# Kernel optimization log

Measured on AMD Instinct MI355X. Metric: run time of the kernel, lower is better.

## Reference

```python
import jax, jax.numpy as jnp
import numpy as np

B, T, N, F = 32, 64, 128, 128
U, K1, K2 = 64, 64, 32
EPS = 1e-3  # keras BatchNormalization default epsilon
SLOPE = 0.01  # LeakyReLU negative_slope


def setup_inputs() -> dict:
    key = jax.random.key(0)
    ks = jax.random.split(key, 16)
    g = lambda k, sh, s=0.05: jax.random.normal(k, sh, dtype=jnp.float32) * s
    inp = {
        "x": jax.random.normal(ks[0], (B, T, F), dtype=jnp.float32),
        "a": jax.random.uniform(ks[1], (B, N, N), dtype=jnp.float32),
        # LSTM (keras gate order i, f, c, o)
        "lstm_k": g(ks[2], (F, 4 * U)),
        "lstm_r": g(ks[3], (U, 4 * U)),
        "lstm_b": jnp.zeros((4 * U,), jnp.float32),
        # BatchNorm params (inference form: gamma, beta, moving mean, moving var)
        "bnl_g": jnp.ones((U,), jnp.float32), "bnl_b": jnp.zeros((U,), jnp.float32),
        "bnl_m": jnp.zeros((U,), jnp.float32), "bnl_v": jnp.ones((U,), jnp.float32),
        "w1": g(ks[4], (U, K1)), "b1": jnp.zeros((K1,), jnp.float32),
        "bn1_g": jnp.ones((K1,), jnp.float32), "bn1_b": jnp.zeros((K1,), jnp.float32),
        "bn1_m": jnp.zeros((K1,), jnp.float32), "bn1_v": jnp.ones((K1,), jnp.float32),
        "w2": g(ks[5], (K1, K2)), "b2": jnp.zeros((K2,), jnp.float32),
        "bn2_g": jnp.ones((K2,), jnp.float32), "bn2_b": jnp.zeros((K2,), jnp.float32),
        "bn2_m": jnp.zeros((K2,), jnp.float32), "bn2_v": jnp.ones((K2,), jnp.float32),
        "d1_w": g(ks[6], (T * N * K2, 3), 0.01), "d1_b": jnp.zeros((3,), jnp.float32),
        "d2_w": g(ks[7], (3, N)), "d2_b": jnp.zeros((N,), jnp.float32),
    }
    return inp


def _bn(x, g, b, m, v):
    return (x - m) * (g * jax.lax.rsqrt(v + EPS)) + b


def _leaky(x):
    return jnp.where(x >= 0, x, SLOPE * x)


def _lstm(x, Wk, Wr, b):
    # x: [B, T, F] -> hs: [B, T, U]
    xz = jnp.einsum('btf,fg->btg', x, Wk) + b  # precompute input projections
    u = Wr.shape[0]
    h0 = jnp.zeros((x.shape[0], u), x.dtype)
    c0 = jnp.zeros((x.shape[0], u), x.dtype)

    def step(carry, zt):
        h, c = carry
        z = zt + h @ Wr
        i, f, g_, o = jnp.split(z, 4, axis=-1)
        i = jax.nn.sigmoid(i); f = jax.nn.sigmoid(f)
        g_ = jnp.tanh(g_); o = jax.nn.sigmoid(o)
        c = f * c + i * g_
        h = o * jnp.tanh(c)
        return (h, c), h

    _, hs = jax.lax.scan(step, (h0, c0), xz.transpose(1, 0, 2))
    return hs.transpose(1, 0, 2)


def reference(x, a, lstm_k, lstm_r, lstm_b, bnl_g, bnl_b, bnl_m, bnl_v,
              w1, b1, bn1_g, bn1_b, bn1_m, bn1_v,
              w2, b2, bn2_g, bn2_b, bn2_m, bn2_v,
              d1_w, d1_b, d2_w, d2_b):
    h = _lstm(x, lstm_k, lstm_r, lstm_b)              # [B, T, U]
    h = _bn(h, bnl_g, bnl_b, bnl_m, bnl_v)            # inference BN; dropout is identity
    # tile each timestep's LSTM output over the N nodes, then GCN1
    support1 = jnp.einsum('btu,uk->btk', h, w1)       # [B, T, K1] (identical across nodes)
    sup1 = jnp.broadcast_to(support1[:, :, None, :], (h.shape[0], h.shape[1], N, w1.shape[1]))
    g1 = jnp.einsum('bij,btjk->btik', a, sup1) + b1   # adjacency matmul
    g1 = _leaky(g1)
    g1 = _bn(g1, bn1_g, bn1_b, bn1_m, bn1_v)
    # GCN2
    sup2 = jnp.einsum('btnk,km->btnm', g1, w2)
    g2 = jnp.einsum('bij,btjm->btim', a, sup2) + b2
    g2 = _leaky(g2)
    g2 = _bn(g2, bn2_g, bn2_b, bn2_m, bn2_v)          # [B, T, N, K2]
    flat = g2.reshape(g2.shape[0], -1)                # [B, T*N*K2]
    d1 = jax.nn.relu(flat @ d1_w + d1_b)              # [B, 3]
    return d1 @ d2_w + d2_b                           # [B, N]
```

## Files before the change

### kernel.cpp

```cpp
#include <hip/hip_runtime.h>

#define BB 32
#define TT 64
#define NN 128
#define FF 128
#define UU 64
#define K1 64
#define K2 32
#define G4 256
#define EPSV 1e-3f
#define SLOPE 0.01f

#define ALD 136
#define SLD 136
#define WLD 72

typedef __attribute__((ext_vector_type(8))) short short8;
typedef __attribute__((ext_vector_type(4))) float f32x4;
typedef __attribute__((ext_vector_type(2))) __fp16 half2v;

__device__ __forceinline__ float sigmoidf_(float x) {
  return __builtin_amdgcn_rcpf(1.f + __expf(-x));
}
__device__ __forceinline__ float tanhf_(float x) {
  return 1.f - 2.f * __builtin_amdgcn_rcpf(__expf(2.f * x) + 1.f);
}
__device__ __forceinline__ float leaky_(float x) { return x >= 0.f ? x : SLOPE * x; }
__device__ __forceinline__ unsigned short f2bf(float x) {
  union { float f; unsigned u; } v; v.f = x;
  unsigned r = v.u + 0x7fff + ((v.u >> 16) & 1);
  return (unsigned short)(r >> 16);
}

__global__ __launch_bounds__(256) void k_pre(const float* __restrict__ x,
                                             const float* __restrict__ wk,
                                             const float* __restrict__ bias,
                                             const float* __restrict__ a,
                                             const float* __restrict__ w2,
                                             const float* __restrict__ wr,
                                             const float* __restrict__ w1,
                                             const float* __restrict__ d1w,
                                             float* __restrict__ xz,
                                             float* __restrict__ rsum,
                                             unsigned short* __restrict__ apad,
                                             unsigned short* __restrict__ w2t,
                                             unsigned* __restrict__ wrp,
                                             unsigned* __restrict__ w1p,
                                             float4* __restrict__ d1r) {
  int tid = threadIdx.x;
  if (blockIdx.x < 32) {
    int b = blockIdx.x;
    int wave = tid >> 6, lane = tid & 63;
    const float* ab = a + (size_t)b * NN * NN;
    for (int r = 0; r < 32; ++r) {
      int row = wave * 32 + r;
      float2 v = *(const float2*)(ab + (size_t)row * NN + lane * 2);
      float s = v.x + v.y;
#pragma unroll
      for (int off = 32; off >= 1; off >>= 1) s += __shfl_down(s, off);
      if (lane == 0) rsum[b * NN + row] = s;
    }
    unsigned short* ap = apad + (size_t)b * NN * ALD;
    for (int idx = tid; idx < NN * NN; idx += 256) {
      int i = idx >> 7, j = idx & 127;
      ap[i * ALD + j] = f2bf(ab[idx]);
    }
    if (b == 0) {
      for (int idx = tid; idx < K1 * K2; idx += 256) {
        int k = idx >> 5, m = idx & 31;
        w2t[m * WLD + k] = f2bf(w2[idx]);
      }
    }
    if (b == 1) {
      for (int idx = tid; idx < 4 * 32 * UU; idx += 256) {
        int u2 = idx & 63;
        int p = (idx >> 6) & 31;
        int gate = idx >> 11;
        int col = gate * UU + u2;
        union { __fp16 h[2]; unsigned u; } pk;
        pk.h[0] = (__fp16)wr[(2 * p) * G4 + col];
        pk.h[1] = (__fp16)wr[(2 * p + 1) * G4 + col];
        wrp[idx] = pk.u;
      }
    }
    if (b == 2) {
      for (int idx = tid; idx < 32 * K1; idx += 256) {
        int k = idx & 63, p = idx >> 6;
        union { __fp16 h[2]; unsigned u; } pk;
        pk.h[0] = (__fp16)w1[(2 * p) * K1 + k];
        pk.h[1] = (__fp16)w1[(2 * p + 1) * K1 + k];
        w1p[idx] = pk.u;
      }
    }
  } else if (blockIdx.x < 288) {
    __shared__ float xs[8][FF];
    int row0 = (blockIdx.x - 32) * 8;
    for (int i = tid; i < 8 * FF; i += 256) xs[i >> 7][i & 127] = x[(size_t)row0 * FF + i];
    __syncthreads();
    int g = tid;
    float acc[8];
    float bg = bias[g];
#pragma unroll
    for (int r = 0; r < 8; ++r) acc[r] = bg;
    for (int f = 0; f < FF; ++f) {
      float w = wk[f * G4 + g];
#pragma unroll
      for (int r = 0; r < 8; ++r) acc[r] += xs[r][f] * w;
    }
#pragma unroll
    for (int r = 0; r < 8; ++r) xz[(size_t)(row0 + r) * G4 + g] = acc[r];
  } else {
    int blk2 = blockIdx.x - 288;
#pragma unroll
    for (int k = 0; k < 4; ++k) {
      int F = (blk2 * 4 + k) * 256 + tid;
      int L = F & 255;
      int rem = F >> 8;
      int c = rem % 3;
      int rem2 = rem / 3;
      int g = rem2 & 3;
      int t = rem2 >> 2;
      int it = g >> 1, mt = g & 1;
      int wv = L >> 6, l = L & 63, l15v = l & 15, l4v = l >> 4;
      int m = mt * 16 + l15v;
      int ibase = (wv * 2 + it) * 16 + l4v * 4;
      float4 v;
      v.x = d1w[((size_t)t * 4096 + (ibase + 0) * 32 + m) * 3 + c];
      v.y = d1w[((size_t)t * 4096 + (ibase + 1) * 32 + m) * 3 + c];
      v.z = d1w[((size_t)t * 4096 + (ibase + 2) * 32 + m) * 3 + c];
      v.w = d1w[((size_t)t * 4096 + (ibase + 3) * 32 + m) * 3 + c];
      d1r[F] = v;
    }
  }
}

__global__ __launch_bounds__(256, 1) void k_lstm(const float* __restrict__ xz,
                                                 const unsigned* __restrict__ wrp,
                                                 const unsigned* __restrict__ w1p,
                                                 const float* __restrict__ bnl_g,
                                                 const float* __restrict__ bnl_b,
                                                 const float* __restrict__ bnl_m,
                                                 const float* __restrict__ bnl_v,
                                                 float* __restrict__ s1out) {
  __shared__ __align__(16) float xz_lds[TT * G4];
  __shared__ __align__(16) __fp16 hp[TT * UU];
  __shared__ __align__(16) __fp16 h16[UU];
  int tid = threadIdx.x;
  int wave = tid >> 6, lane = tid & 63;
  int b = blockIdx.x;

  {
    const float4* src = (const float4*)(xz + (size_t)b * TT * G4);
    float4* dst = (float4*)xz_lds;
#pragma unroll
    for (int k = 0; k < 16; ++k) dst[tid + k * 256] = src[tid + k * 256];
  }
  unsigned w1v[32];
#pragma unroll
  for (int p = 0; p < 32; ++p) w1v[p] = w1p[p * 64 + lane];

  float bscale = bnl_g[lane] * rsqrtf(bnl_v[lane] + EPSV);
  float boff = bnl_b[lane] - bnl_m[lane] * bscale;

  unsigned wv[4][32];
  if (wave == 0) {
#pragma unroll
    for (int gate = 0; gate < 4; ++gate)
#pragma unroll
      for (int p = 0; p < 32; ++p) wv[gate][p] = wrp[(gate * 32 + p) * UU + lane];
    h16[lane] = (__fp16)0.f;
  }
  __syncthreads();

  if (wave == 0) {
    float c = 0.f;
    for (int t = 0; t < TT; ++t) {
      unsigned hw[32];
      {
        const uint4* hq = (const uint4*)h16;
#pragma unroll
        for (int k = 0; k < 8; ++k) {
          uint4 v = hq[k];
          hw[4 * k + 0] = v.x; hw[4 * k + 1] = v.y; hw[4 * k + 2] = v.z; hw[4 * k + 3] = v.w;
        }
      }
      float zi = xz_lds[t * G4 + lane];
      float zf = xz_lds[t * G4 + 64 + lane];
      float zg = xz_lds[t * G4 + 128 + lane];
      float zo = xz_lds[t * G4 + 192 + lane];
#pragma unroll
      for (int p = 0; p < 32; ++p) {
        half2v hh = __builtin_bit_cast(half2v, hw[p]);
        zi = __builtin_amdgcn_fdot2(__builtin_bit_cast(half2v, wv[0][p]), hh, zi, false);
        zf = __builtin_amdgcn_fdot2(__builtin_bit_cast(half2v, wv[1][p]), hh, zf, false);
        zg = __builtin_amdgcn_fdot2(__builtin_bit_cast(half2v, wv[2][p]), hh, zg, false);
        zo = __builtin_amdgcn_fdot2(__builtin_bit_cast(half2v, wv[3][p]), hh, zo, false);
      }
      float i_ = sigmoidf_(zi), f_ = sigmoidf_(zf), g_ = tanhf_(zg), o_ = sigmoidf_(zo);
      c = f_ * c + i_ * g_;
      float h = o_ * tanhf_(c);
      h16[lane] = (__fp16)h;
      hp[t * UU + lane] = (__fp16)(h * bscale + boff);
    }
  }
  __syncthreads();

  float* s1b = s1out + (size_t)b * TT * K1;
  for (int r = 0; r < 16; ++r) {
    int t = wave * 16 + r;
    unsigned hw2[32];
    {
      const uint4* hq = (const uint4*)(hp + t * UU);
#pragma unroll
      for (int k = 0; k < 8; ++k) {
        uint4 v = hq[k];
        hw2[4 * k + 0] = v.x; hw2[4 * k + 1] = v.y; hw2[4 * k + 2] = v.z; hw2[4 * k + 3] = v.w;
      }
    }
    float acc = 0.f;
#pragma unroll
    for (int p = 0; p < 32; ++p)
      acc = __builtin_amdgcn_fdot2(__builtin_bit_cast(half2v, w1v[p]),
                                   __builtin_bit_cast(half2v, hw2[p]), acc, false);
    s1b[t * K1 + lane] = acc;
  }
}

__global__ __launch_bounds__(256) void k_gcn(
    const float* __restrict__ s1g, const float* __restrict__ rsum,
    const unsigned short* __restrict__ apad, const unsigned short* __restrict__ w2t,
    const float* __restrict__ b1,
    const float* __restrict__ bn1_g, const float* __restrict__ bn1_b,
    const float* __restrict__ bn1_m, const float* __restrict__ bn1_v,
    const float* __restrict__ b2,
    const float* __restrict__ bn2_g, const float* __restrict__ bn2_b,
    const float* __restrict__ bn2_m, const float* __restrict__ bn2_v,
    const float4* __restrict__ d1r, float* __restrict__ part) {
  __shared__ unsigned short a_lds[NN * ALD];
  __shared__ unsigned short s2_lds[K2 * SLD];
  __shared__ unsigned short w2_lds[K2 * WLD];
  __shared__ float4 gp[K1];
  __shared__ float r_lds[NN];
  __shared__ float p2[3 * K2];
  __shared__ float red[12];

  int blk = blockIdx.x;
  int b = blk & 31, t = blk >> 5;
  int tid = threadIdx.x;
  int lane = tid & 63, wave = tid >> 6;
  int l15 = lane & 15, l4 = lane >> 4;

  {
    const uint4* src = (const uint4*)(apad + (size_t)b * NN * ALD);
    uint4* dst = (uint4*)a_lds;
    for (int i = tid; i < NN * ALD / 8; i += 256) dst[i] = src[i];
  }
  {
    const uint2* src = (const uint2*)w2t;
    uint2* dst = (uint2*)w2_lds;
    for (int i = tid; i < K2 * WLD / 4; i += 256) dst[i] = src[i];
  }
  if (tid < K1) {
    float s1v = s1g[((size_t)b * TT + t) * K1 + tid];
    float s = bn1_g[tid] * rsqrtf(bn1_v[tid] + EPSV);
    gp[tid] = make_float4(s1v, b1[tid], s, bn1_b[tid] - bn1_m[tid] * s);
  }
  if (tid >= 64 && tid < 64 + NN) r_lds[tid - 64] = rsum[b * NN + (tid - 64)];
  if (tid >= 192 && tid < 192 + K2) {
    int m = tid - 192;
    float s = bn2_g[m] * rsqrtf(bn2_v[m] + EPSV);
    p2[m] = b2[m];
    p2[K2 + m] = s;
    p2[2 * K2 + m] = bn2_b[m] - bn2_m[m] * s;
  }
  __syncthreads();

  f32x4 z4 = {0.f, 0.f, 0.f, 0.f};

  {
    float rj0 = r_lds[(wave * 2 + 0) * 16 + l15];
    float rj1 = r_lds[(wave * 2 + 1) * 16 + l15];
    f32x4 acc[2][2];
    acc[0][0] = z4; acc[0][1] = z4; acc[1][0] = z4; acc[1][1] = z4;
#pragma unroll
    for (int kt = 0; kt < 2; ++kt) {
      float4 gpv[8];
#pragma unroll
      for (int e = 0; e < 8; ++e) gpv[e] = gp[kt * 32 + l4 * 8 + e];
      short8 bfrag0 = *((const short8*)&w2_lds[(0 + l15) * WLD + kt * 32 + l4 * 8]);
      short8 bfrag1 = *((const short8*)&w2_lds[(16 + l15) * WLD + kt * 32 + l4 * 8]);
#pragma unroll
      for (int jt = 0; jt < 2; ++jt) {
        float rj = jt ? rj1 : rj0;
        short8 af;
#pragma unroll
        for (int e = 0; e < 8; ++e) {
          float4 p = gpv[e];
          float v = leaky_(rj * p.x + p.y) * p.z + p.w;
          af[e] = (short)f2bf(v);
        }
        acc[jt][0] = __builtin_amdgcn_mfma_f32_16x16x32_bf16(af, bfrag0, acc[jt][0], 0, 0, 0);
        acc[jt][1] = __builtin_amdgcn_mfma_f32_16x16x32_bf16(af, bfrag1, acc[jt][1], 0, 0, 0);
      }
    }
#pragma unroll
    for (int jt = 0; jt < 2; ++jt) {
      int jbase = (wave * 2 + jt) * 16 + l4 * 4;
#pragma unroll
      for (int mt = 0; mt < 2; ++mt) {
        int m = mt * 16 + l15;
        unsigned lo = (unsigned)f2bf(acc[jt][mt][0]) | ((unsigned)f2bf(acc[jt][mt][1]) << 16);
        unsigned hi = (unsigned)f2bf(acc[jt][mt][2]) | ((unsigned)f2bf(acc[jt][mt][3]) << 16);
        uint2 val; val.x = lo; val.y = hi;
        *((uint2*)&s2_lds[m * SLD + jbase]) = val;
      }
    }
  }
  __syncthreads();

  float c0 = 0.f, c1 = 0.f, c2 = 0.f;
  {
    f32x4 acc[2][2];
    acc[0][0] = z4; acc[0][1] = z4; acc[1][0] = z4; acc[1][1] = z4;
#pragma unroll
    for (int kt = 0; kt < 4; ++kt) {
      short8 bfrag0 = *((const short8*)&s2_lds[(0 + l15) * SLD + kt * 32 + l4 * 8]);
      short8 bfrag1 = *((const short8*)&s2_lds[(16 + l15) * SLD + kt * 32 + l4 * 8]);
#pragma unroll
      for (int it = 0; it < 2; ++it) {
        int i = (wave * 2 + it) * 16 + l15;
        short8 afrag = *((const short8*)&a_lds[i * ALD + kt * 32 + l4 * 8]);
        acc[it][0] = __builtin_amdgcn_mfma_f32_16x16x32_bf16(afrag, bfrag0, acc[it][0], 0, 0, 0);
        acc[it][1] = __builtin_amdgcn_mfma_f32_16x16x32_bf16(afrag, bfrag1, acc[it][1], 0, 0, 0);
      }
    }
    float gv[2][2][4];
#pragma unroll
    for (int it = 0; it < 2; ++it)
#pragma unroll
      for (int mt = 0; mt < 2; ++mt) {
        int m = mt * 16 + l15;
        float bb = p2[m], bs = p2[K2 + m], bo = p2[2 * K2 + m];
#pragma unroll
        for (int r = 0; r < 4; ++r) gv[it][mt][r] = leaky_(acc[it][mt][r] + bb) * bs + bo;
      }
#pragma unroll
    for (int g = 0; g < 4; ++g) {
      int it = g >> 1, mt = g & 1;
      float4 v0 = d1r[(((size_t)t * 4 + g) * 3 + 0) * 256 + tid];
      float4 v1 = d1r[(((size_t)t * 4 + g) * 3 + 1) * 256 + tid];
      float4 v2 = d1r[(((size_t)t * 4 + g) * 3 + 2) * 256 + tid];
      c0 += gv[it][mt][0] * v0.x + gv[it][mt][1] * v0.y + gv[it][mt][2] * v0.z + gv[it][mt][3] * v0.w;
      c1 += gv[it][mt][0] * v1.x + gv[it][mt][1] * v1.y + gv[it][mt][2] * v1.z + gv[it][mt][3] * v1.w;
      c2 += gv[it][mt][0] * v2.x + gv[it][mt][1] * v2.y + gv[it][mt][2] * v2.z + gv[it][mt][3] * v2.w;
    }
  }
#pragma unroll
  for (int off = 32; off >= 1; off >>= 1) {
    c0 += __shfl_down(c0, off);
    c1 += __shfl_down(c1, off);
    c2 += __shfl_down(c2, off);
  }
  if (lane == 0) { red[wave * 3 + 0] = c0; red[wave * 3 + 1] = c1; red[wave * 3 + 2] = c2; }
  __syncthreads();
  if (tid == 0) {
    float s0 = 0.f, s1v = 0.f, s2v = 0.f;
    for (int w = 0; w < 4; ++w) { s0 += red[w * 3]; s1v += red[w * 3 + 1]; s2v += red[w * 3 + 2]; }
    part[((size_t)b * TT + t) * 3 + 0] = s0;
    part[((size_t)b * TT + t) * 3 + 1] = s1v;
    part[((size_t)b * TT + t) * 3 + 2] = s2v;
  }
}

__global__ __launch_bounds__(128) void k_out(const float* __restrict__ part,
                                             const float* __restrict__ d1b,
                                             const float* __restrict__ d2w,
                                             const float* __restrict__ d2b,
                                             float* __restrict__ out) {
  int b = blockIdx.x, n = threadIdx.x;
  float s[3] = {0.f, 0.f, 0.f};
  const float* p = part + (size_t)b * TT * 3;
  for (int t = 0; t < TT; ++t) {
    s[0] += p[t * 3];
    s[1] += p[t * 3 + 1];
    s[2] += p[t * 3 + 2];
  }
  float o = d2b[n];
#pragma unroll
  for (int c = 0; c < 3; ++c) {
    float d = s[c] + d1b[c];
    d = d > 0.f ? d : 0.f;
    o += d * d2w[c * NN + n];
  }
  out[b * NN + n] = o;
}

extern "C" void kernel_launch(void* const* d_in, const int* in_sizes, int n_in,
                              void* d_out, int out_size, void* d_ws, size_t ws_size,
                              hipStream_t stream) {
  const float* x      = (const float*)d_in[0];
  const float* a      = (const float*)d_in[1];
  const float* lstm_k = (const float*)d_in[2];
  const float* lstm_r = (const float*)d_in[3];
  const float* lstm_b = (const float*)d_in[4];
  const float* bnl_g  = (const float*)d_in[5];
  const float* bnl_b  = (const float*)d_in[6];
  const float* bnl_m  = (const float*)d_in[7];
  const float* bnl_v  = (const float*)d_in[8];
  const float* w1     = (const float*)d_in[9];
  const float* b1     = (const float*)d_in[10];
  const float* bn1_g  = (const float*)d_in[11];
  const float* bn1_b  = (const float*)d_in[12];
  const float* bn1_m  = (const float*)d_in[13];
  const float* bn1_v  = (const float*)d_in[14];
  const float* w2     = (const float*)d_in[15];
  const float* b2     = (const float*)d_in[16];
  const float* bn2_g  = (const float*)d_in[17];
  const float* bn2_b  = (const float*)d_in[18];
  const float* bn2_m  = (const float*)d_in[19];
  const float* bn2_v  = (const float*)d_in[20];
  const float* d1_w   = (const float*)d_in[21];
  const float* d1_b   = (const float*)d_in[22];
  const float* d2_w   = (const float*)d_in[23];
  const float* d2_b   = (const float*)d_in[24];
  float* out = (float*)d_out;

  char* ws = (char*)d_ws;
  float* xz            = (float*)(ws + 0);
  float* s1            = (float*)(ws + 2097152);
  float* rsum          = (float*)(ws + 2621440);
  float* part          = (float*)(ws + 2637824);
  unsigned short* apad = (unsigned short*)(ws + 2662400);
  unsigned short* w2t  = (unsigned short*)(ws + 3776512);
  unsigned* wrp        = (unsigned*)(ws + 3781120);
  unsigned* w1p        = (unsigned*)(ws + 3813888);
  float4* d1r          = (float4*)(ws + 3822080);

  k_pre<<<480, 256, 0, stream>>>(x, lstm_k, lstm_b, a, w2, lstm_r, w1, d1_w,
                                 xz, rsum, apad, w2t, wrp, w1p, d1r);
  k_lstm<<<BB, 256, 0, stream>>>(xz, wrp, w1p, bnl_g, bnl_b, bnl_m, bnl_v, s1);
  k_gcn<<<BB * TT, 256, 0, stream>>>(s1, rsum, apad, w2t, b1, bn1_g, bn1_b, bn1_m, bn1_v,
                                     b2, bn2_g, bn2_b, bn2_m, bn2_v, d1r, part);
  k_out<<<BB, 128, 0, stream>>>(part, d1_b, d2_w, d2_b, out);
}
```

Baseline: 82.19 us.

## Pack eight LSTM sequences per block, prefetch xz from global, restage d1 weight transpose

The LSTM kernel now runs one batch sequence per wave, eight waves per 512-thread block, on 4 blocks. It drops the LDS copy of xz and instead prefetches the next timestep's gate inputs from global memory into registers. The recurrent and w1 weight packings are transposed so each lane loads its weights with contiguous uint4 reads. The d1 weight reorder in k_pre now goes through LDS in coalesced chunks, one block per timestep, which cuts the pre-kernel grid from 480 to 352 blocks. Concentrating 32 sequences on only 4 CUs trades parallel spread for fewer launched blocks, and each step now depends on global load latency instead of LDS.

Result: slower. 117.3 us (+42.8%).

```diff
diff --git a/kernel.cpp b/kernel.cpp
--- a/kernel.cpp
+++ b/kernel.cpp
@@ -73,10 +73,10 @@
     }
     if (b == 1) {
       for (int idx = tid; idx < 4 * 32 * UU; idx += 256) {
-        int u2 = idx & 63;
-        int p = (idx >> 6) & 31;
-        int gate = idx >> 11;
-        int col = gate * UU + u2;
+        int p = idx & 31;
+        int gate = (idx >> 5) & 3;
+        int u = idx >> 7;
+        int col = gate * UU + u;
         union { __fp16 h[2]; unsigned u; } pk;
         pk.h[0] = (__fp16)wr[(2 * p) * G4 + col];
         pk.h[1] = (__fp16)wr[(2 * p + 1) * G4 + col];
@@ -85,7 +85,7 @@
     }
     if (b == 2) {
       for (int idx = tid; idx < 32 * K1; idx += 256) {
-        int k = idx & 63, p = idx >> 6;
+        int p = idx & 31, k = idx >> 5;
         union { __fp16 h[2]; unsigned u; } pk;
         pk.h[0] = (__fp16)w1[(2 * p) * K1 + k];
         pk.h[1] = (__fp16)w1[(2 * p + 1) * K1 + k];
@@ -110,31 +110,36 @@
 #pragma unroll
     for (int r = 0; r < 8; ++r) xz[(size_t)(row0 + r) * G4 + g] = acc[r];
   } else {
-    int blk2 = blockIdx.x - 288;
-#pragma unroll
-    for (int k = 0; k < 4; ++k) {
-      int F = (blk2 * 4 + k) * 256 + tid;
-      int L = F & 255;
-      int rem = F >> 8;
-      int c = rem % 3;
-      int rem2 = rem / 3;
-      int g = rem2 & 3;
-      int t = rem2 >> 2;
-      int it = g >> 1, mt = g & 1;
-      int wv = L >> 6, l = L & 63, l15v = l & 15, l4v = l >> 4;
-      int m = mt * 16 + l15v;
-      int ibase = (wv * 2 + it) * 16 + l4v * 4;
-      float4 v;
-      v.x = d1w[((size_t)t * 4096 + (ibase + 0) * 32 + m) * 3 + c];
-      v.y = d1w[((size_t)t * 4096 + (ibase + 1) * 32 + m) * 3 + c];
-      v.z = d1w[((size_t)t * 4096 + (ibase + 2) * 32 + m) * 3 + c];
-      v.w = d1w[((size_t)t * 4096 + (ibase + 3) * 32 + m) * 3 + c];
-      d1r[F] = v;
-    }
-  }
-}
-
-__global__ __launch_bounds__(256, 1) void k_lstm(const float* __restrict__ xz,
+    int t = blockIdx.x - 288;
+    __shared__ float dt[3072];
+    const float* src = d1w + (size_t)t * NN * K2 * 3;
+    for (int c32 = 0; c32 < 4; ++c32) {
+      __syncthreads();
+      for (int i = tid; i < 768; i += 256)
+        ((float4*)dt)[i] = ((const float4*)(src + c32 * 3072))[i];
+      __syncthreads();
+#pragma unroll
+      for (int q = 0; q < 3; ++q) {
+        int item = q * 256 + tid;
+        int l = item & 63;
+        int gc = item >> 6;
+        int g = gc / 3, c = gc % 3;
+        int it = g >> 1, mt = g & 1;
+        int l15v = l & 15, l4v = l >> 4;
+        int m = mt * 16 + l15v;
+        int rowbase = it * 16 + l4v * 4;
+        float4 v;
+        v.x = dt[(rowbase + 0) * 96 + m * 3 + c];
+        v.y = dt[(rowbase + 1) * 96 + m * 3 + c];
+        v.z = dt[(rowbase + 2) * 96 + m * 3 + c];
+        v.w = dt[(rowbase + 3) * 96 + m * 3 + c];
+        d1r[(((size_t)t * 4 + g) * 3 + c) * 256 + c32 * 64 + l] = v;
+      }
+    }
+  }
+}
+
+__global__ __launch_bounds__(512, 2) void k_lstm(const float* __restrict__ xz,
                                                  const unsigned* __restrict__ wrp,
                                                  const unsigned* __restrict__ w1p,
                                                  const float* __restrict__ bnl_g,
@@ -142,75 +147,76 @@
                                                  const float* __restrict__ bnl_m,
                                                  const float* __restrict__ bnl_v,
                                                  float* __restrict__ s1out) {
-  __shared__ __align__(16) float xz_lds[TT * G4];
-  __shared__ __align__(16) __fp16 hp[TT * UU];
-  __shared__ __align__(16) __fp16 h16[UU];
+  __shared__ __align__(16) __fp16 hp[8][TT * UU];
+  __shared__ __align__(16) __fp16 h16[8][UU];
   int tid = threadIdx.x;
   int wave = tid >> 6, lane = tid & 63;
-  int b = blockIdx.x;
-
-  {
-    const float4* src = (const float4*)(xz + (size_t)b * TT * G4);
-    float4* dst = (float4*)xz_lds;
-#pragma unroll
-    for (int k = 0; k < 16; ++k) dst[tid + k * 256] = src[tid + k * 256];
-  }
-  unsigned w1v[32];
-#pragma unroll
-  for (int p = 0; p < 32; ++p) w1v[p] = w1p[p * 64 + lane];
-
+  int b = blockIdx.x * 8 + wave;
+
+  unsigned wv[4][32];
+  {
+    const uint4* wp = (const uint4*)(wrp + (size_t)lane * 128);
+#pragma unroll
+    for (int k = 0; k < 32; ++k) {
+      uint4 v = wp[k];
+      int gate = k >> 3, p0 = (k & 7) * 4;
+      wv[gate][p0 + 0] = v.x; wv[gate][p0 + 1] = v.y;
+      wv[gate][p0 + 2] = v.z; wv[gate][p0 + 3] = v.w;
+    }
+  }
   float bscale = bnl_g[lane] * rsqrtf(bnl_v[lane] + EPSV);
   float boff = bnl_b[lane] - bnl_m[lane] * bscale;
-
-  unsigned wv[4][32];
-  if (wave == 0) {
-#pragma unroll
-    for (int gate = 0; gate < 4; ++gate)
-#pragma unroll
-      for (int p = 0; p < 32; ++p) wv[gate][p] = wrp[(gate * 32 + p) * UU + lane];
-    h16[lane] = (__fp16)0.f;
-  }
-  __syncthreads();
-
-  if (wave == 0) {
-    float c = 0.f;
-    for (int t = 0; t < TT; ++t) {
-      unsigned hw[32];
-      {
-        const uint4* hq = (const uint4*)h16;
-#pragma unroll
-        for (int k = 0; k < 8; ++k) {
-          uint4 v = hq[k];
-          hw[4 * k + 0] = v.x; hw[4 * k + 1] = v.y; hw[4 * k + 2] = v.z; hw[4 * k + 3] = v.w;
-        }
-      }
-      float zi = xz_lds[t * G4 + lane];
-      float zf = xz_lds[t * G4 + 64 + lane];
-      float zg = xz_lds[t * G4 + 128 + lane];
-      float zo = xz_lds[t * G4 + 192 + lane];
-#pragma unroll
-      for (int p = 0; p < 32; ++p) {
-        half2v hh = __builtin_bit_cast(half2v, hw[p]);
-        zi = __builtin_amdgcn_fdot2(__builtin_bit_cast(half2v, wv[0][p]), hh, zi, false);
-        zf = __builtin_amdgcn_fdot2(__builtin_bit_cast(half2v, wv[1][p]), hh, zf, false);
-        zg = __builtin_amdgcn_fdot2(__builtin_bit_cast(half2v, wv[2][p]), hh, zg, false);
-        zo = __builtin_amdgcn_fdot2(__builtin_bit_cast(half2v, wv[3][p]), hh, zo, false);
-      }
-      float i_ = sigmoidf_(zi), f_ = sigmoidf_(zf), g_ = tanhf_(zg), o_ = sigmoidf_(zo);
-      c = f_ * c + i_ * g_;
-      float h = o_ * tanhf_(c);
-      h16[lane] = (__fp16)h;
-      hp[t * UU + lane] = (__fp16)(h * bscale + boff);
-    }
-  }
-  __syncthreads();
-
+  h16[wave][lane] = (__fp16)0.f;
+  float c = 0.f;
+
+  const float* xzb = xz + (size_t)b * TT * G4;
+  __fp16* hpw = &hp[wave][0];
+  float czi = xzb[lane], czf = xzb[64 + lane], czg = xzb[128 + lane], czo = xzb[192 + lane];
+
+  for (int t = 0; t < TT; ++t) {
+    int tn = (t + 1 < TT) ? t + 1 : t;
+    const float* nb = xzb + tn * G4;
+    float nzi = nb[lane], nzf = nb[64 + lane], nzg = nb[128 + lane], nzo = nb[192 + lane];
+    unsigned hw[32];
+    {
+      const uint4* hq = (const uint4*)&h16[wave][0];
+#pragma unroll
+      for (int k = 0; k < 8; ++k) {
+        uint4 v = hq[k];
+        hw[4 * k + 0] = v.x; hw[4 * k + 1] = v.y; hw[4 * k + 2] = v.z; hw[4 * k + 3] = v.w;
+      }
+    }
+    float zi = czi, zf = czf, zg = czg, zo = czo;
+#pragma unroll
+    for (int p = 0; p < 32; ++p) {
+      half2v hh = __builtin_bit_cast(half2v, hw[p]);
+      zi = __builtin_amdgcn_fdot2(__builtin_bit_cast(half2v, wv[0][p]), hh, zi, false);
+      zf = __builtin_amdgcn_fdot2(__builtin_bit_cast(half2v, wv[1][p]), hh, zf, false);
+      zg = __builtin_amdgcn_fdot2(__builtin_bit_cast(half2v, wv[2][p]), hh, zg, false);
+      zo = __builtin_amdgcn_fdot2(__builtin_bit_cast(half2v, wv[3][p]), hh, zo, false);
+    }
+    float i_ = sigmoidf_(zi), f_ = sigmoidf_(zf), g_ = tanhf_(zg), o_ = sigmoidf_(zo);
+    c = f_ * c + i_ * g_;
+    float h = o_ * tanhf_(c);
+    h16[wave][lane] = (__fp16)h;
+    hpw[t * UU + lane] = (__fp16)(h * bscale + boff);
+    czi = nzi; czf = nzf; czg = nzg; czo = nzo;
+  }
+
+  unsigned w1v[32];
+  {
+    const uint4* wp1 = (const uint4*)(w1p + (size_t)lane * 32);
+#pragma unroll
+    for (int k = 0; k < 8; ++k) {
+      uint4 v = wp1[k];
+      w1v[4 * k + 0] = v.x; w1v[4 * k + 1] = v.y; w1v[4 * k + 2] = v.z; w1v[4 * k + 3] = v.w;
+    }
+  }
   float* s1b = s1out + (size_t)b * TT * K1;
-  for (int r = 0; r < 16; ++r) {
-    int t = wave * 16 + r;
+  for (int t = 0; t < TT; ++t) {
     unsigned hw2[32];
     {
-      const uint4* hq = (const uint4*)(hp + t * UU);
+      const uint4* hq = (const uint4*)(hpw + t * UU);
 #pragma unroll
       for (int k = 0; k < 8; ++k) {
         uint4 v = hq[k];
@@ -436,9 +442,9 @@
   unsigned* w1p        = (unsigned*)(ws + 3813888);
   float4* d1r          = (float4*)(ws + 3822080);
 
-  k_pre<<<480, 256, 0, stream>>>(x, lstm_k, lstm_b, a, w2, lstm_r, w1, d1_w,
+  k_pre<<<352, 256, 0, stream>>>(x, lstm_k, lstm_b, a, w2, lstm_r, w1, d1_w,
                                  xz, rsum, apad, w2t, wrp, w1p, d1r);
-  k_lstm<<<BB, 256, 0, stream>>>(xz, wrp, w1p, bnl_g, bnl_b, bnl_m, bnl_v, s1);
+  k_lstm<<<4, 512, 0, stream>>>(xz, wrp, w1p, bnl_g, bnl_b, bnl_m, bnl_v, s1);
   k_gcn<<<BB * TT, 256, 0, stream>>>(s1, rsum, apad, w2t, b1, bn1_g, bn1_b, bn1_m, bn1_v,
                                      b2, bn2_g, bn2_b, bn2_m, bn2_v, d1r, part);
   k_out<<<BB, 128, 0, stream>>>(part, d1_b, d2_w, d2_b, out);
```
